# Performance work log

Measured on AMD Instinct MI355X. Metric: run time of the kernel, lower is better.

The kernel has to match this reference:

```python
import jax, jax.numpy as jnp
import numpy as np
from jax import lax

HEADS = 8
L, B, D, H, V, T = 128, 16, 512, 512, 16000, 32


def setup_inputs() -> dict:
    key = jax.random.key(0)
    ks = jax.random.split(key, 16)
    p = lambda k, shape, fan: (jax.random.normal(k, shape, jnp.float32) * (fan ** -0.5))
    output_len = jnp.sort(jax.random.randint(ks[15], (B,), 1, T + 1))[::-1]
    output_len = output_len.at[0].set(T)  # max(output_len) == T, sorted descending
    return dict(
        memory=jax.random.normal(ks[0], (L, B, D), jnp.float32),
        emb=p(ks[1], (V, H), H),
        Wq=p(ks[2], (2 * H, H), 2 * H), bq=jnp.zeros((H,), jnp.float32),
        Wk=p(ks[3], (D, H), D), bk=jnp.zeros((H,), jnp.float32),
        Wv=p(ks[4], (D, H), D), bv=jnp.zeros((H,), jnp.float32),
        W_ih=p(ks[5], (H, 3 * H), H), b_ih=p(ks[6], (3 * H,), H),
        W_hh=p(ks[7], (H, 3 * H), H), b_hh=p(ks[8], (3 * H,), H),
        Wf=p(ks[9], (H, V), H), bf=jnp.zeros((V,), jnp.float32),
        output_len=output_len.astype(jnp.int32),
        max_output_len=T,
    )


def _forward(memory, emb, Wq, bq, Wk, bk, Wv, bv, W_ih, b_ih, W_hh, b_hh, Wf, bf,
             output_len, max_output_len):
    Lm, bs, _ = memory.shape
    Hh = emb.shape[1]
    dk = Hh // HEADS
    scale = 1.0 / np.sqrt(dk)

    def mha(query):  # query: (1, bs, 2H); recomputes k/v projections each step (faithful)
        qh = (query @ Wq + bq).reshape(1, bs, HEADS, dk).transpose(2, 1, 0, 3)   # (h,b,1,dk)
        kh = (memory @ Wk + bk).reshape(Lm, bs, HEADS, dk).transpose(2, 1, 0, 3)  # (h,b,L,dk)
        vh = (memory @ Wv + bv).reshape(Lm, bs, HEADS, dk).transpose(2, 1, 0, 3)
        score = jax.nn.softmax(jnp.einsum('hbqd,hbkd->hbqk', qh, kh) * scale, axis=-1)
        ctx = jnp.einsum('hbqk,hbkd->hbqd', score, vh)          # (h,b,1,dk)
        ctx = ctx.transpose(2, 1, 0, 3).reshape(1, bs, Hh)       # (1,b,H)
        sc = score.transpose(2, 1, 0, 3).mean(axis=2)            # (1,b,L) mean over heads
        return ctx, sc

    def gru_cell(x, h):  # (bs,H),(bs,H) -> (bs,H); PyTorch GRU equations
        gi = x @ W_ih + b_ih
        gh = h @ W_hh + b_hh
        ir, iz, inn = jnp.split(gi, 3, axis=-1)
        hr, hz, hn = jnp.split(gh, 3, axis=-1)
        r = jax.nn.sigmoid(ir + hr)
        z = jax.nn.sigmoid(iz + hz)
        n = jnp.tanh(inn + r * hn)
        return (1.0 - z) * n + z * h

    def step(carry, i):
        out, hid = carry  # (bs,V), (bs,H)
        embedded = emb[jnp.argmax(out, axis=-1)]                 # (bs,H)
        query = jnp.concatenate([embedded, hid], axis=-1)[None]  # (1,bs,2H)
        ctx, sc = mha(query)
        h_new = gru_cell(ctx[0], hid)
        logits = h_new @ Wf + bf                                 # fc on GRU output
        # masking replaces torch's shrinking-batch slicing (output_len sorted desc)
        active = (i < output_len)[:, None].astype(logits.dtype)
        return (logits, h_new), (logits * active, h_new * active, sc[0] * active)

    init = (jnp.zeros((bs, Wf.shape[1]), memory.dtype), jnp.zeros((bs, Hh), memory.dtype))
    _, (outputs, hiddens, scores) = lax.scan(step, init, jnp.arange(max_output_len))
    return outputs, hiddens, scores


def reference(memory, emb, Wq, bq, Wk, bk, Wv, bv, W_ih, b_ih, W_hh, b_hh, Wf, bf,
              output_len, max_output_len):
    return _forward(memory, emb, Wq, bq, Wk, bk, Wv, bv, W_ih, b_ih, W_hh, b_hh,
                    Wf, bf, output_len, max_output_len)
```

## Files before the change

### kernel.cpp

```cpp
#include <hip/hip_runtime.h>

#define LL 128
#define BB 16
#define HH 512
#define VV 16000
#define TT 32
#define NH 8
#define DK 64

#define WS_K 0
#define WS_V (LL*BB*HH)
#define WS_HID0 (2*LL*BB*HH)
#define WS_HID1 (WS_HID0 + BB*HH)
#define WS_CTX  (WS_HID1 + BB*HH)
#define WS_P    (WS_CTX + BB*HH)
#define WS_HS   (WS_P + BB*NH*LL)
#define WS_SLOTS_F (WS_HS + 6*BB*HH)
#define WS_WFP (WS_SLOTS_F + 2*(TT+1)*BB + 16)

#define OUT_HID_OFF ((size_t)TT*BB*VV)
#define OUT_SC_OFF  (OUT_HID_OFF + (size_t)TT*BB*HH)


__global__ __launch_bounds__(256) void kv_kernel(const float* __restrict__ mem,
        const float* __restrict__ Wk, const float* __restrict__ bk,
        const float* __restrict__ Wv, const float* __restrict__ bv,
        const float* __restrict__ Wf, float* __restrict__ ws) {
    int blk = blockIdx.x;
    int tid = threadIdx.x;

    if (blk >= 2048) {
        int m = blk - 2048;
        int colb = m * 32;
        float* dst = ws + WS_WFP + (size_t)m*16384;
        #pragma unroll
        for (int j = 0; j < 16; ++j) {
            int i = tid + 256*j;
            int k = i >> 3, c4 = i & 7;
            float4 v = *(const float4*)(Wf + (size_t)k*VV + colb + c4*4);
            *(float4*)(dst + (size_t)k*32 + c4*4) = v;
        }
        return;
    }

    int rg = blk >> 4, ct = blk & 15;
    int isV = ct >= 8;
    int colbase = (ct & 7) * 64;
    const float* W = isV ? Wv : Wk;
    const float* bias = isV ? bv : bk;
    float* outp = ws + (isV ? WS_V : WS_K);
    int rowbase = rg * 16;
    __shared__ float As[16*516];

    {
        const float4* srcp = (const float4*)(mem + (size_t)rowbase*512);
        #pragma unroll
        for (int j = 0; j < 8; ++j) {
            int i = tid + 256*j;
            float4 v = srcp[i];
            int row = i >> 7, c4i = i & 127;
            *(float4*)(As + row*516 + c4i*4) = v;
        }
    }
    if (blk == 0) {
        for (int i = tid; i < BB*HH; i += 256) ws[WS_HID0 + i] = 0.f;
        unsigned long long* slots = (unsigned long long*)(ws + WS_SLOTS_F);
        for (int i = tid; i < (TT+1)*BB; i += 256)
            slots[i] = (i < BB) ? 0xFFFFFFFFull : 0ull;
    }
    __syncthreads();

    int cq = tid & 15;
    int rq4 = (tid >> 4) & 3;
    int kq = tid >> 6;
    float acc[4][4];
    #pragma unroll
    for (int i = 0; i < 4; ++i) { acc[i][0]=0.f; acc[i][1]=0.f; acc[i][2]=0.f; acc[i][3]=0.f; }
    const float* wp = W + colbase + cq*4;
    for (int k4 = kq*32; k4 < kq*32 + 32; ++k4) {
        float4 a0 = *(const float4*)(As + (rq4*4+0)*516 + k4*4);
        float4 a1 = *(const float4*)(As + (rq4*4+1)*516 + k4*4);
        float4 a2 = *(const float4*)(As + (rq4*4+2)*516 + k4*4);
        float4 a3 = *(const float4*)(As + (rq4*4+3)*516 + k4*4);
        const float* wrow = wp + (size_t)(4*k4)*512;
        float4 w0 = *(const float4*)(wrow);
        float4 w1 = *(const float4*)(wrow + 512);
        float4 w2 = *(const float4*)(wrow + 1024);
        float4 w3 = *(const float4*)(wrow + 1536);
        #define KV_FMA(ri, A) \
            acc[ri][0] += A.x*w0.x + A.y*w1.x + A.z*w2.x + A.w*w3.x; \
            acc[ri][1] += A.x*w0.y + A.y*w1.y + A.z*w2.y + A.w*w3.y; \
            acc[ri][2] += A.x*w0.z + A.y*w1.z + A.z*w2.z + A.w*w3.z; \
            acc[ri][3] += A.x*w0.w + A.y*w1.w + A.z*w2.w + A.w*w3.w;
        KV_FMA(0, a0) KV_FMA(1, a1) KV_FMA(2, a2) KV_FMA(3, a3)
        #undef KV_FMA
    }
    __syncthreads();
    float* red = As;
    #pragma unroll
    for (int ri = 0; ri < 4; ++ri)
        *(float4*)(red + ri*1024 + tid*4) =
            make_float4(acc[ri][0], acc[ri][1], acc[ri][2], acc[ri][3]);
    __syncthreads();
    {
        int c4 = tid & 15, row = tid >> 4;
        int rq = row >> 2, ri = row & 3;
        float4 b4v = *(const float4*)(bias + colbase + c4*4);
        float o[4] = {b4v.x, b4v.y, b4v.z, b4v.w};
        #pragma unroll
        for (int kq2 = 0; kq2 < 4; ++kq2) {
            const float* pr = red + ri*1024 + (kq2*64 + rq*16 + c4)*4;
            o[0] += pr[0]; o[1] += pr[1]; o[2] += pr[2]; o[3] += pr[3];
        }
        *(float4*)(outp + (size_t)(rowbase + row)*512 + colbase + c4*4) =
            make_float4(o[0], o[1], o[2], o[3]);
    }
}

__global__ __launch_bounds__(256) void attn_kernel(
        const float* __restrict__ emb, const float* __restrict__ Wq,
        const float* __restrict__ bq, float* __restrict__ ws, int t) {
    int b = blockIdx.x >> 3, h = blockIdx.x & 7;
    int tid = threadIdx.x;
    const float* hid = ws + ((t & 1) ? WS_HID1 : WS_HID0);
    unsigned long long* slots = (unsigned long long*)(ws + WS_SLOTS_F);
    __shared__ float q[2*HH];
    __shared__ float part[8*64];
    __shared__ float qh[64];
    __shared__ float sp[2*LL];
    __shared__ float p[LL];
    __shared__ float cpart[4*64];

    unsigned long long slot = slots[t*BB + b];
    unsigned idx = 0xFFFFFFFFu - (unsigned)(slot & 0xFFFFFFFFull);
    for (int i = tid; i < HH; i += 256) {
        q[i] = emb[(size_t)idx*HH + i];
        q[HH + i] = hid[b*HH + i];
    }
    __syncthreads();

    {
        int c2 = tid & 31, kc = tid >> 5;
        const float* wp = Wq + (size_t)(kc*128)*HH + h*64 + c2*2;
        const float* qp = q + kc*128;
        float a0 = 0.f, a1 = 0.f;
        #pragma unroll 8
        for (int kk = 0; kk < 128; ++kk) {
            float x = qp[kk];
            float2 w2 = *(const float2*)(wp + (size_t)kk*HH);
            a0 += x*w2.x; a1 += x*w2.y;
        }
        part[kc*64 + c2*2]     = a0;
        part[kc*64 + c2*2 + 1] = a1;
    }
    __syncthreads();
    if (tid < 64) {
        float s = bq[h*64 + tid];
        #pragma unroll
        for (int kc = 0; kc < 8; ++kc) s += part[kc*64 + tid];
        qh[tid] = s;
    }
    __syncthreads();

    {
        int l = tid & 127, jh = tid >> 7;
        const float4* kr = (const float4*)(ws + WS_K + ((size_t)(l*BB + b))*HH + h*DK) + jh*8;
        const float4* q4 = (const float4*)qh + jh*8;
        float acc = 0.f;
        #pragma unroll
        for (int j = 0; j < 8; ++j) {
            float4 kv = kr[j], qq = q4[j];
            acc += qq.x*kv.x + qq.y*kv.y + qq.z*kv.z + qq.w*kv.w;
        }
        sp[jh*128 + l] = acc;
    }
    __syncthreads();

    if (tid < 64) {
        float s0 = (sp[tid]      + sp[128 + tid]) * 0.125f;
        float s1 = (sp[64 + tid] + sp[192 + tid]) * 0.125f;
        float m = fmaxf(s0, s1);
        #pragma unroll
        for (int off = 32; off; off >>= 1) m = fmaxf(m, __shfl_xor(m, off));
        float e0 = expf(s0 - m), e1 = expf(s1 - m);
        float sum = e0 + e1;
        #pragma unroll
        for (int off = 32; off; off >>= 1) sum += __shfl_xor(sum, off);
        float inv = 1.f / sum;
        p[tid]      = e0 * inv;
        p[64 + tid] = e1 * inv;
    }
    __syncthreads();
    if (tid < 128) ws[WS_P + (size_t)(b*NH + h)*LL + tid] = p[tid];

    {
        int c = tid & 63, lc = tid >> 6;
        const float* Vp = ws + WS_V + h*DK + c;
        float acc = 0.f;
        #pragma unroll 8
        for (int li = 0; li < 32; ++li) {
            int l = lc*32 + li;
            acc += p[l] * Vp[(size_t)(l*BB + b)*HH];
        }
        cpart[lc*64 + c] = acc;
    }
    __syncthreads();
    if (tid < 64)
        ws[WS_CTX + b*HH + h*DK + tid] =
            cpart[tid] + cpart[64+tid] + cpart[128+tid] + cpart[192+tid];
}

__global__ __launch_bounds__(512) void gates_kernel(
        const float* __restrict__ Wih, const float* __restrict__ bih,
        const float* __restrict__ Whh, const float* __restrict__ bhh,
        const int* __restrict__ olen, float* __restrict__ ws,
        float* __restrict__ out, int t) {
    int cb = blockIdx.x;
    int tid = threadIdx.x;
    const float* hid_in = ws + ((t & 1) ? WS_HID1 : WS_HID0);
    float* hid_out = ws + ((t & 1) ? WS_HID0 : WS_HID1);
    const float* ctx = ws + WS_CTX;
    __shared__ float xs[512*20];
    __shared__ float hh[512*20];
    __shared__ float part[8*256];
    __shared__ float gacc[6*256];

    for (int i = tid; i < BB*HH; i += 512) {
        int bb = i >> 9, k = i & 511;
        xs[k*20 + bb] = ctx[i];
        hh[k*20 + bb] = hid_in[i];
    }
    if (tid < 64) {
        int e = cb*64 + tid;
        int b = e >> 7, l = e & 127;
        float s = 0.f;
        #pragma unroll
        for (int hq = 0; hq < NH; ++hq)
            s += ws[WS_P + (size_t)(b*NH + hq)*LL + l];
        out[OUT_SC_OFF + ((size_t)t*BB + b)*LL + l] = (t < olen[b]) ? s*0.125f : 0.f;
    }
    __syncthreads();

    int c4 = tid & 3, b4 = (tid >> 2) & 3, kc = tid >> 4;
    int wv = tid >> 6;
    for (int g = 0; g < 6; ++g) {
        const float* W = (g < 3) ? Wih : Whh;
        int gg = (g < 3) ? g : g - 3;
        const float* xsrc = (g < 3) ? xs : hh;
        const float* wp = W + (size_t)kc*(3*HH) + gg*HH + cb*16 + c4*4;
        const float* xp = xsrc + kc*20 + b4*4;
        float acc[4][4];
        #pragma unroll
        for (int i = 0; i < 4; ++i) { acc[i][0]=0.f; acc[i][1]=0.f; acc[i][2]=0.f; acc[i][3]=0.f; }
        #pragma unroll 8
        for (int i = 0; i < 16; ++i) {
            float4 w4 = *(const float4*)wp;
            float4 x4 = *(const float4*)xp;
            wp += (size_t)32*(3*HH);
            xp += 32*20;
            acc[0][0] += x4.x*w4.x; acc[0][1] += x4.x*w4.y; acc[0][2] += x4.x*w4.z; acc[0][3] += x4.x*w4.w;
            acc[1][0] += x4.y*w4.x; acc[1][1] += x4.y*w4.y; acc[1][2] += x4.y*w4.z; acc[1][3] += x4.y*w4.w;
            acc[2][0] += x4.z*w4.x; acc[2][1] += x4.z*w4.y; acc[2][2] += x4.z*w4.z; acc[2][3] += x4.z*w4.w;
            acc[3][0] += x4.w*w4.x; acc[3][1] += x4.w*w4.y; acc[3][2] += x4.w*w4.z; acc[3][3] += x4.w*w4.w;
        }
        #pragma unroll
        for (int bi = 0; bi < 4; ++bi)
            #pragma unroll
            for (int ci = 0; ci < 4; ++ci) {
                float v = acc[bi][ci];
                v += __shfl_xor(v, 16);
                v += __shfl_xor(v, 32);
                acc[bi][ci] = v;
            }
        if ((tid & 48) == 0) {
            #pragma unroll
            for (int bi = 0; bi < 4; ++bi)
                *(float4*)(part + wv*256 + (b4*4+bi)*16 + c4*4) =
                    make_float4(acc[bi][0], acc[bi][1], acc[bi][2], acc[bi][3]);
        }
        __syncthreads();
        if (tid < 256) {
            int b = tid >> 4, c = tid & 15;
            float s = 0.f;
            #pragma unroll
            for (int w = 0; w < 8; ++w) s += part[w*256 + b*16 + c];
            gacc[g*256 + b*16 + c] = s;
        }
        __syncthreads();
    }

    if (tid < 256) {
        int b = tid >> 4, c = tid & 15;
        int col = cb*16 + c;
        float gir = gacc[0*256 + b*16 + c] + bih[col];
        float giz = gacc[1*256 + b*16 + c] + bih[HH + col];
        float gin = gacc[2*256 + b*16 + c] + bih[2*HH + col];
        float ghr = gacc[3*256 + b*16 + c] + bhh[col];
        float ghz = gacc[4*256 + b*16 + c] + bhh[HH + col];
        float ghn = gacc[5*256 + b*16 + c] + bhh[2*HH + col];
        float r = 1.f/(1.f + __expf(-(gir + ghr)));
        float z = 1.f/(1.f + __expf(-(giz + ghz)));
        float xn = gin + r*ghn;
        float n = 1.f - 2.f/(__expf(2.f*xn) + 1.f);
        float hprev = hh[col*20 + b];
        float hnew = (1.f - z)*n + z*hprev;
        hid_out[b*HH + col] = hnew;
        out[OUT_HID_OFF + ((size_t)t*BB + b)*HH + col] = (t < olen[b]) ? hnew : 0.f;
        ws[WS_HS + col*16 + b] = hnew;
    }
}

__global__ __launch_bounds__(256) void logits_kernel(
        const float* __restrict__ bf, const int* __restrict__ olen,
        float* __restrict__ ws, float* __restrict__ out, int t) {
    __shared__ float hs[HH*20];
    __shared__ float red[4*512];
    __shared__ unsigned long long am[BB*16];
    int tid = threadIdx.x;

    {
        const float4* s4 = (const float4*)(ws + WS_HS);
        #pragma unroll
        for (int j = 0; j < 8; ++j) {
            int i = tid + 256*j;
            float4 v = s4[i];
            int row = i >> 2, qo = i & 3;
            *(float4*)(hs + row*20 + qo*4) = v;
        }
    }
    __syncthreads();

    int c4 = tid & 7, kc = tid >> 3;
    int colbase = blockIdx.x * 32;
    const float* wtile = ws + WS_WFP + (size_t)blockIdx.x*16384;
    float acc[16][4];
    #pragma unroll
    for (int bi = 0; bi < 16; ++bi) { acc[bi][0]=0.f; acc[bi][1]=0.f; acc[bi][2]=0.f; acc[bi][3]=0.f; }
    const float* wp = wtile + (size_t)kc*32 + c4*4;
    const float* hp = hs + kc*20;
    #pragma unroll 8
    for (int i = 0; i < 16; ++i) {
        float4 w4 = *(const float4*)wp;
        float4 h0 = *(const float4*)(hp);
        float4 h1 = *(const float4*)(hp + 4);
        float4 h2 = *(const float4*)(hp + 8);
        float4 h3 = *(const float4*)(hp + 12);
        wp += 32 * 32;
        hp += 32 * 20;
        #define LACC(bi, hv) acc[bi][0] += (hv)*w4.x; acc[bi][1] += (hv)*w4.y; \
                             acc[bi][2] += (hv)*w4.z; acc[bi][3] += (hv)*w4.w;
        LACC(0,h0.x)  LACC(1,h0.y)  LACC(2,h0.z)  LACC(3,h0.w)
        LACC(4,h1.x)  LACC(5,h1.y)  LACC(6,h1.z)  LACC(7,h1.w)
        LACC(8,h2.x)  LACC(9,h2.y)  LACC(10,h2.z) LACC(11,h2.w)
        LACC(12,h3.x) LACC(13,h3.y) LACC(14,h3.z) LACC(15,h3.w)
        #undef LACC
    }

    #pragma unroll
    for (int bi = 0; bi < 16; ++bi)
        #pragma unroll
        for (int ci = 0; ci < 4; ++ci) {
            float v = acc[bi][ci];
            v += __shfl_xor(v, 8);
            v += __shfl_xor(v, 16);
            v += __shfl_xor(v, 32);
            acc[bi][ci] = v;
        }
    int wv = tid >> 6;
    if ((tid & 56) == 0) {
        #pragma unroll
        for (int bi = 0; bi < 16; ++bi)
            *(float4*)(red + wv*512 + bi*32 + c4*4) =
                make_float4(acc[bi][0], acc[bi][1], acc[bi][2], acc[bi][3]);
    }
    __syncthreads();

    {
        int b = tid >> 4, cp = (tid & 15) * 2;
        float2 bf2 = *(const float2*)(bf + colbase + cp);
        float v0 = bf2.x, v1 = bf2.y;
        #pragma unroll
        for (int w = 0; w < 4; ++w) {
            v0 += red[w*512 + b*32 + cp];
            v1 += red[w*512 + b*32 + cp + 1];
        }
        bool active = t < olen[b];
        float2 ov; ov.x = active ? v0 : 0.f; ov.y = active ? v1 : 0.f;
        *(float2*)(out + ((size_t)t*BB + b)*VV + colbase + cp) = ov;

        unsigned u0 = __float_as_uint(v0);
        u0 = (u0 & 0x80000000u) ? ~u0 : (u0 | 0x80000000u);
        unsigned u1 = __float_as_uint(v1);
        u1 = (u1 & 0x80000000u) ? ~u1 : (u1 | 0x80000000u);
        unsigned long long e0 = ((unsigned long long)u0 << 32)
                              | (unsigned long long)(0xFFFFFFFFu - (unsigned)(colbase + cp));
        unsigned long long e1 = ((unsigned long long)u1 << 32)
                              | (unsigned long long)(0xFFFFFFFFu - (unsigned)(colbase + cp + 1));
        am[b*16 + (tid & 15)] = e0 > e1 ? e0 : e1;
    }
    __syncthreads();
    if (tid < BB) {
        unsigned long long m = 0ull;
        #pragma unroll
        for (int i = 0; i < 16; ++i) {
            unsigned long long v = am[tid*16 + i];
            m = v > m ? v : m;
        }
        unsigned long long* slots = (unsigned long long*)(ws + WS_SLOTS_F);
        atomicMax(&slots[(size_t)(t+1)*BB + tid], m);
    }
}

extern "C" void kernel_launch(void* const* d_in, const int* in_sizes, int n_in,
                              void* d_out, int out_size, void* d_ws, size_t ws_size,
                              hipStream_t stream) {
    const float* mem = (const float*)d_in[0];
    const float* emb = (const float*)d_in[1];
    const float* Wq  = (const float*)d_in[2];
    const float* bq  = (const float*)d_in[3];
    const float* Wk  = (const float*)d_in[4];
    const float* bk  = (const float*)d_in[5];
    const float* Wv  = (const float*)d_in[6];
    const float* bv  = (const float*)d_in[7];
    const float* Wih = (const float*)d_in[8];
    const float* bih = (const float*)d_in[9];
    const float* Whh = (const float*)d_in[10];
    const float* bhh = (const float*)d_in[11];
    const float* Wf  = (const float*)d_in[12];
    const float* bf  = (const float*)d_in[13];
    const int* olen  = (const int*)d_in[14];
    float* out = (float*)d_out;
    float* ws  = (float*)d_ws;

    hipLaunchKernelGGL(kv_kernel, dim3(2548), dim3(256), 0, stream,
                       mem, Wk, bk, Wv, bv, Wf, ws);
    for (int t = 0; t < TT; ++t) {
        hipLaunchKernelGGL(attn_kernel, dim3(BB*NH), dim3(256), 0, stream, emb, Wq, bq, ws, t);
        hipLaunchKernelGGL(gates_kernel, dim3(32), dim3(512), 0, stream,
                           Wih, bih, Whh, bhh, olen, ws, out, t);
        hipLaunchKernelGGL(logits_kernel, dim3(500), dim3(256), 0, stream,
                           bf, olen, ws, out, t);
    }
}
```

Baseline: 1.428 ms.

## Replace atomic argmax slots with per-block candidates and fuse GRU gate passes

The logits kernel now writes each block's per-batch argmax candidate to a dedicated array instead of calling atomicMax on a shared per-step slot. The attention kernel reduces the 500 candidates itself with a wave shuffle. The Wq projection loop is reworked into float4 loads with shuffle reduction. The GRU gates kernel computes the r/z/n gates together in two passes instead of six, sharing the x loads. The aim is to remove global atomic contention and repeated shared-memory input reads, at the cost of more registers and a larger shared partial buffer in the gates kernel.

```diff
diff --git a/kernel.cpp b/kernel.cpp
--- a/kernel.cpp
+++ b/kernel.cpp
@@ -15,11 +15,14 @@
 #define WS_CTX  (WS_HID1 + BB*HH)
 #define WS_P    (WS_CTX + BB*HH)
 #define WS_HS   (WS_P + BB*NH*LL)
-#define WS_SLOTS_F (WS_HS + 6*BB*HH)
-#define WS_WFP (WS_SLOTS_F + 2*(TT+1)*BB + 16)
+#define WS_CAND (WS_HS + BB*HH + 16)
+#define WS_WFP  (WS_CAND + 2*512*BB)
 
 #define OUT_HID_OFF ((size_t)TT*BB*VV)
 #define OUT_SC_OFF  (OUT_HID_OFF + (size_t)TT*BB*HH)
+
+typedef unsigned long long u64;
+__device__ __forceinline__ u64 u64max(u64 a, u64 b) { return a > b ? a : b; }
 
 
 __global__ __launch_bounds__(256) void kv_kernel(const float* __restrict__ mem,
@@ -64,9 +67,8 @@
     }
     if (blk == 0) {
         for (int i = tid; i < BB*HH; i += 256) ws[WS_HID0 + i] = 0.f;
-        unsigned long long* slots = (unsigned long long*)(ws + WS_SLOTS_F);
-        for (int i = tid; i < (TT+1)*BB; i += 256)
-            slots[i] = (i < BB) ? 0xFFFFFFFFull : 0ull;
+        u64* cand = (u64*)(ws + WS_CAND);
+        for (int i = tid; i < 512*BB; i += 256) cand[i] = 0ull;
     }
     __syncthreads();
 
@@ -123,16 +125,29 @@
     int b = blockIdx.x >> 3, h = blockIdx.x & 7;
     int tid = threadIdx.x;
     const float* hid = ws + ((t & 1) ? WS_HID1 : WS_HID0);
-    unsigned long long* slots = (unsigned long long*)(ws + WS_SLOTS_F);
     __shared__ float q[2*HH];
-    __shared__ float part[8*64];
+    __shared__ float part[4*64];
     __shared__ float qh[64];
     __shared__ float sp[2*LL];
     __shared__ float p[LL];
     __shared__ float cpart[4*64];
-
-    unsigned long long slot = slots[t*BB + b];
-    unsigned idx = 0xFFFFFFFFu - (unsigned)(slot & 0xFFFFFFFFull);
+    __shared__ unsigned idx_s;
+
+    if (t > 0) {
+        if (tid < 64) {
+            const u64* cp = (const u64*)(ws + WS_CAND) + b;
+            u64 m = 0ull;
+            #pragma unroll
+            for (int j = 0; j < 8; ++j)
+                m = u64max(m, cp[(size_t)(tid + 64*j)*BB]);
+            #pragma unroll
+            for (int off = 32; off; off >>= 1)
+                m = u64max(m, (u64)__shfl_xor((long long)m, off));
+            if (tid == 0) idx_s = 0xFFFFFFFFu - (unsigned)(m & 0xFFFFFFFFull);
+        }
+    } else if (tid == 0) idx_s = 0u;
+    __syncthreads();
+    unsigned idx = idx_s;
     for (int i = tid; i < HH; i += 256) {
         q[i] = emb[(size_t)idx*HH + i];
         q[HH + i] = hid[b*HH + i];
@@ -140,24 +155,30 @@
     __syncthreads();
 
     {
-        int c2 = tid & 31, kc = tid >> 5;
-        const float* wp = Wq + (size_t)(kc*128)*HH + h*64 + c2*2;
-        const float* qp = q + kc*128;
-        float a0 = 0.f, a1 = 0.f;
+        int c4 = tid & 15, kc = tid >> 4;
+        const float* wp = Wq + (size_t)kc*HH + h*64 + c4*4;
+        float ax=0.f, ay=0.f, az=0.f, aw=0.f;
         #pragma unroll 8
-        for (int kk = 0; kk < 128; ++kk) {
-            float x = qp[kk];
-            float2 w2 = *(const float2*)(wp + (size_t)kk*HH);
-            a0 += x*w2.x; a1 += x*w2.y;
-        }
-        part[kc*64 + c2*2]     = a0;
-        part[kc*64 + c2*2 + 1] = a1;
+        for (int i = 0; i < 64; ++i) {
+            float x = q[kc + 16*i];
+            float4 w4 = *(const float4*)wp;
+            wp += (size_t)16*HH;
+            ax += x*w4.x; ay += x*w4.y; az += x*w4.z; aw += x*w4.w;
+        }
+        float v;
+        v = ax; v += __shfl_xor(v,16); v += __shfl_xor(v,32); ax = v;
+        v = ay; v += __shfl_xor(v,16); v += __shfl_xor(v,32); ay = v;
+        v = az; v += __shfl_xor(v,16); v += __shfl_xor(v,32); az = v;
+        v = aw; v += __shfl_xor(v,16); v += __shfl_xor(v,32); aw = v;
+        int wv = tid >> 6;
+        if ((tid & 48) == 0)
+            *(float4*)(part + wv*64 + c4*4) = make_float4(ax, ay, az, aw);
     }
     __syncthreads();
     if (tid < 64) {
         float s = bq[h*64 + tid];
         #pragma unroll
-        for (int kc = 0; kc < 8; ++kc) s += part[kc*64 + tid];
+        for (int wv = 0; wv < 4; ++wv) s += part[wv*64 + tid];
         qh[tid] = s;
     }
     __syncthreads();
@@ -222,7 +243,7 @@
     const float* ctx = ws + WS_CTX;
     __shared__ float xs[512*20];
     __shared__ float hh[512*20];
-    __shared__ float part[8*256];
+    __shared__ float part[3*8*256];
     __shared__ float gacc[6*256];
 
     for (int i = tid; i < BB*HH; i += 512) {
@@ -243,48 +264,59 @@
 
     int c4 = tid & 3, b4 = (tid >> 2) & 3, kc = tid >> 4;
     int wv = tid >> 6;
-    for (int g = 0; g < 6; ++g) {
-        const float* W = (g < 3) ? Wih : Whh;
-        int gg = (g < 3) ? g : g - 3;
-        const float* xsrc = (g < 3) ? xs : hh;
-        const float* wp = W + (size_t)kc*(3*HH) + gg*HH + cb*16 + c4*4;
+    #pragma unroll
+    for (int pass = 0; pass < 2; ++pass) {
+        const float* W = pass ? Whh : Wih;
+        const float* xsrc = pass ? hh : xs;
+        float aR[4][4], aZ[4][4], aN[4][4];
+        #pragma unroll
+        for (int i = 0; i < 4; ++i)
+            #pragma unroll
+            for (int j = 0; j < 4; ++j) { aR[i][j]=0.f; aZ[i][j]=0.f; aN[i][j]=0.f; }
+        const float* wp = W + (size_t)kc*(3*HH) + cb*16 + c4*4;
         const float* xp = xsrc + kc*20 + b4*4;
-        float acc[4][4];
-        #pragma unroll
-        for (int i = 0; i < 4; ++i) { acc[i][0]=0.f; acc[i][1]=0.f; acc[i][2]=0.f; acc[i][3]=0.f; }
-        #pragma unroll 8
+        #pragma unroll 4
         for (int i = 0; i < 16; ++i) {
-            float4 w4 = *(const float4*)wp;
+            float4 wr = *(const float4*)(wp);
+            float4 wz = *(const float4*)(wp + HH);
+            float4 wn = *(const float4*)(wp + 2*HH);
             float4 x4 = *(const float4*)xp;
             wp += (size_t)32*(3*HH);
             xp += 32*20;
-            acc[0][0] += x4.x*w4.x; acc[0][1] += x4.x*w4.y; acc[0][2] += x4.x*w4.z; acc[0][3] += x4.x*w4.w;
-            acc[1][0] += x4.y*w4.x; acc[1][1] += x4.y*w4.y; acc[1][2] += x4.y*w4.z; acc[1][3] += x4.y*w4.w;
-            acc[2][0] += x4.z*w4.x; acc[2][1] += x4.z*w4.y; acc[2][2] += x4.z*w4.z; acc[2][3] += x4.z*w4.w;
-            acc[3][0] += x4.w*w4.x; acc[3][1] += x4.w*w4.y; acc[3][2] += x4.w*w4.z; acc[3][3] += x4.w*w4.w;
+            #define GR(bi, xv) \
+                aR[bi][0] += xv*wr.x; aR[bi][1] += xv*wr.y; aR[bi][2] += xv*wr.z; aR[bi][3] += xv*wr.w; \
+                aZ[bi][0] += xv*wz.x; aZ[bi][1] += xv*wz.y; aZ[bi][2] += xv*wz.z; aZ[bi][3] += xv*wz.w; \
+                aN[bi][0] += xv*wn.x; aN[bi][1] += xv*wn.y; aN[bi][2] += xv*wn.z; aN[bi][3] += xv*wn.w;
+            GR(0, x4.x) GR(1, x4.y) GR(2, x4.z) GR(3, x4.w)
+            #undef GR
         }
         #pragma unroll
         for (int bi = 0; bi < 4; ++bi)
             #pragma unroll
             for (int ci = 0; ci < 4; ++ci) {
-                float v = acc[bi][ci];
-                v += __shfl_xor(v, 16);
-                v += __shfl_xor(v, 32);
-                acc[bi][ci] = v;
+                float v;
+                v = aR[bi][ci]; v += __shfl_xor(v,16); v += __shfl_xor(v,32); aR[bi][ci] = v;
+                v = aZ[bi][ci]; v += __shfl_xor(v,16); v += __shfl_xor(v,32); aZ[bi][ci] = v;
+                v = aN[bi][ci]; v += __shfl_xor(v,16); v += __shfl_xor(v,32); aN[bi][ci] = v;
             }
         if ((tid & 48) == 0) {
             #pragma unroll
-            for (int bi = 0; bi < 4; ++bi)
-                *(float4*)(part + wv*256 + (b4*4+bi)*16 + c4*4) =
-                    make_float4(acc[bi][0], acc[bi][1], acc[bi][2], acc[bi][3]);
+            for (int bi = 0; bi < 4; ++bi) {
+                *(float4*)(part + (0*8 + wv)*256 + (b4*4+bi)*16 + c4*4) =
+                    make_float4(aR[bi][0], aR[bi][1], aR[bi][2], aR[bi][3]);
+                *(float4*)(part + (1*8 + wv)*256 + (b4*4+bi)*16 + c4*4) =
+                    make_float4(aZ[bi][0], aZ[bi][1], aZ[bi][2], aZ[bi][3]);
+                *(float4*)(part + (2*8 + wv)*256 + (b4*4+bi)*16 + c4*4) =
+                    make_float4(aN[bi][0], aN[bi][1], aN[bi][2], aN[bi][3]);
+            }
         }
         __syncthreads();
-        if (tid < 256) {
-            int b = tid >> 4, c = tid & 15;
+        for (int e2 = tid; e2 < 768; e2 += 512) {
+            int g = e2 >> 8, e = e2 & 255;
             float s = 0.f;
             #pragma unroll
-            for (int w = 0; w < 8; ++w) s += part[w*256 + b*16 + c];
-            gacc[g*256 + b*16 + c] = s;
+            for (int w = 0; w < 8; ++w) s += part[(g*8 + w)*256 + e];
+            gacc[(pass*3 + g)*256 + e] = s;
         }
         __syncthreads();
     }
@@ -315,7 +347,7 @@
         float* __restrict__ ws, float* __restrict__ out, int t) {
     __shared__ float hs[HH*20];
     __shared__ float red[4*512];
-    __shared__ unsigned long long am[BB*16];
+    __shared__ u64 am[BB*16];
     int tid = threadIdx.x;
 
     {
@@ -392,22 +424,19 @@
         u0 = (u0 & 0x80000000u) ? ~u0 : (u0 | 0x80000000u);
         unsigned u1 = __float_as_uint(v1);
         u1 = (u1 & 0x80000000u) ? ~u1 : (u1 | 0x80000000u);
-        unsigned long long e0 = ((unsigned long long)u0 << 32)
-                              | (unsigned long long)(0xFFFFFFFFu - (unsigned)(colbase + cp));
-        unsigned long long e1 = ((unsigned long long)u1 << 32)
-                              | (unsigned long long)(0xFFFFFFFFu - (unsigned)(colbase + cp + 1));
+        u64 e0 = ((u64)u0 << 32) | (u64)(0xFFFFFFFFu - (unsigned)(colbase + cp));
+        u64 e1 = ((u64)u1 << 32) | (u64)(0xFFFFFFFFu - (unsigned)(colbase + cp + 1));
         am[b*16 + (tid & 15)] = e0 > e1 ? e0 : e1;
     }
     __syncthreads();
     if (tid < BB) {
-        unsigned long long m = 0ull;
+        u64 m = 0ull;
         #pragma unroll
         for (int i = 0; i < 16; ++i) {
-            unsigned long long v = am[tid*16 + i];
+            u64 v = am[tid*16 + i];
             m = v > m ? v : m;
         }
-        unsigned long long* slots = (unsigned long long*)(ws + WS_SLOTS_F);
-        atomicMax(&slots[(size_t)(t+1)*BB + tid], m);
+        ((u64*)(ws + WS_CAND))[(size_t)blockIdx.x*BB + tid] = m;
     }
 }
 
```

New measurement: 1.250 ms. -12.4%, faster.
